# Performance work log

Measured on AMD Instinct MI355X. Metric: run time of the kernel, lower is better.

The kernel has to match this reference:

```python
import jax, jax.numpy as jnp
import numpy as np

MUL = 32      # multiplicity of each irrep type: 32x0e + 32x1o (dim = 32 + 96 = 128)
NSPEC = 10
NGRAPH = 16
EPS = 1e-5


def _split(x):
    # x: [N, 128] -> scalars [N, 32], vectors [N, 32, 3]
    return x[:, :MUL], x[:, MUL:].reshape(x.shape[0], MUL, 3)


def _cat(s, v):
    return jnp.concatenate([s, v.reshape(v.shape[0], MUL * 3)], axis=1)


def _irreps_linear(s, v, w0, w1, b0=None):
    # e3nn o3.Linear: per-irrep-type multiplicity mixing, /sqrt(fan_in), bias on scalars only
    inv = 1.0 / np.sqrt(MUL)
    s2 = s @ w0 * inv
    if b0 is not None:
        s2 = s2 + b0
    v2 = jnp.einsum('nuc,uw->nwc', v, w1) * inv
    return s2, v2


def _tensor_product(s1, v1, s2, v2, w000, w110, w011, w101):
    # SeparateWeightTensorProduct with per-path internal weights, lmax=1 paths:
    #   0e x 0e -> 0e, 1o x 1o -> 0e (CG = delta/sqrt(3)), 0e x 1o -> 1o, 1o x 0e -> 1o
    inv = 1.0 / np.sqrt(MUL * MUL)
    half = 1.0 / np.sqrt(2.0)  # two paths feed each output irrep
    out0 = (jnp.einsum('nu,nv,uvw->nw', s1, s2, w000)
            + jnp.einsum('nuc,nvc,uvw->nw', v1, v2, w110) / np.sqrt(3.0)) * (inv * half)
    out1 = (jnp.einsum('nu,nvc,uvw->nwc', s1, v2, w011)
            + jnp.einsum('nuc,nv,uvw->nwc', v1, s2, w101)) * (inv * half)
    return out0, out1


def _e3_layer_norm(s, v, batch, ln_w0, ln_b0, ln_w1):
    # per-graph equivariant layer norm: subtract mean on scalars, RMS-normalize each irrep field
    ones = jnp.ones(batch.shape, s.dtype)
    cnt = jnp.maximum(jax.ops.segment_sum(ones, batch, NGRAPH), 1.0)
    mean = jax.ops.segment_sum(s.sum(-1), batch, NGRAPH) / (cnt * MUL)
    s = s - mean[batch][:, None]
    n2s = jax.ops.segment_sum((s * s).sum(-1), batch, NGRAPH) / (cnt * MUL)
    s = s * jax.lax.rsqrt(n2s + EPS)[batch][:, None] * ln_w0 + ln_b0
    n2v = jax.ops.segment_sum((v * v).sum((-1, -2)), batch, NGRAPH) / (cnt * MUL)
    v = v * jax.lax.rsqrt(n2v + EPS)[batch][:, None, None] * ln_w1[None, :, None]
    return s, v


def setup_inputs() -> dict:
    key = jax.random.key(0)
    ks = jax.random.split(key, 24)
    N, B = 50000, 2
    rn = lambda k, sh: jax.random.normal(k, sh, dtype=jnp.float32)
    inp = {
        'node_feats_hidden': rn(ks[0], (B, N, MUL * 4)),
        'node_feats_up': rn(ks[1], (N, MUL * 4)),
        'hl_w0': rn(ks[2], (B, MUL, MUL)), 'hl_w1': rn(ks[3], (B, MUL, MUL)),
        'ul_w0': rn(ks[4], (B, MUL, MUL)), 'ul_w1': rn(ks[5], (B, MUL, MUL)),
        'tp_w000': rn(ks[6], (B, MUL, MUL, MUL)), 'tp_w110': rn(ks[7], (B, MUL, MUL, MUL)),
        'tp_w011': rn(ks[8], (B, MUL, MUL, MUL)), 'tp_w101': rn(ks[9], (B, MUL, MUL, MUL)),
        'lp_w0': rn(ks[10], (B, MUL, MUL)), 'lp_b0': jnp.zeros((B, MUL), jnp.float32),
        'lp_w1': rn(ks[11], (B, MUL, MUL)),
        'sc_w0': rn(ks[12], (B, MUL, NSPEC, MUL)), 'sc_w1': rn(ks[13], (B, MUL, NSPEC, MUL)),
        'ln_w0': jnp.ones((B, MUL), jnp.float32), 'ln_b0': jnp.zeros((B, MUL), jnp.float32),
        'ln_w1': jnp.ones((B, MUL), jnp.float32),
        'sk_w0': rn(ks[14], (B, MUL, MUL)), 'sk_b0': jnp.zeros((B, MUL), jnp.float32),
        'sk_w1': rn(ks[15], (B, MUL, MUL)),
        'node_species': jax.random.randint(ks[16], (N,), 0, NSPEC),
        'batch': jnp.sort(jax.random.randint(ks[17], (N,), 0, NGRAPH)),
    }
    return inp


def reference(node_feats_hidden, node_feats_up, hl_w0, hl_w1, ul_w0, ul_w1,
              tp_w000, tp_w110, tp_w011, tp_w101, lp_w0, lp_b0, lp_w1,
              sc_w0, sc_w1, ln_w0, ln_b0, ln_w1, sk_w0, sk_b0, sk_w1,
              node_species, batch):
    oh = jax.nn.one_hot(node_species, NSPEC, dtype=node_feats_up.dtype)
    inv_sc = 1.0 / np.sqrt(MUL * NSPEC)
    up = node_feats_up
    outs = []
    for b in range(node_feats_hidden.shape[0]):  # num_interactions blocks (fixed, small)
        sh, vh = _split(node_feats_hidden[b])
        su, vu = _split(up)
        shp, vhp = _irreps_linear(sh, vh, hl_w0[b], hl_w1[b])
        sup, vup = _irreps_linear(su, vu, ul_w0[b], ul_w1[b])
        z0, z1 = _tensor_product(shp, vhp, sup, vup,
                                 tp_w000[b], tp_w110[b], tp_w011[b], tp_w101[b])
        z0, z1 = _irreps_linear(z0, z1, lp_w0[b], lp_w1[b], lp_b0[b])
        # self connection: FullyConnectedTensorProduct(hidden, one-hot '10x0e', out)
        z0 = z0 + jnp.einsum('nu,nv,uvw->nw', sh, oh, sc_w0[b]) * inv_sc
        z1 = z1 + jnp.einsum('nuc,nv,uvw->nwc', vh, oh, sc_w1[b]) * inv_sc
        z0, z1 = _e3_layer_norm(z0, z1, batch, ln_w0[b], ln_b0[b], ln_w1[b])
        sk0, sk1 = _irreps_linear(sh, vh, sk_w0[b], sk_w1[b], sk_b0[b])
        out = _cat(z0 + sk0, z1 + sk1)
        outs.append(out)
        up = out  # next block consumes this block's output as node_feats_up
    return jnp.stack(outs)
```

## Files before the change

kernel.cpp:

```cpp
#include <hip/hip_runtime.h>
#include <math.h>

#define MULT 32
#define NSPEC 10
#define NGRAPH 16
#define NBANK 64
#define NCBANK 16
#define INV_SC 0.05590169943749474f
#define INV32S 0.17677669529663687f

typedef unsigned short u16;
typedef __bf16 v8bf __attribute__((ext_vector_type(8)));
typedef float v4f __attribute__((ext_vector_type(4)));
typedef unsigned int v4u_t __attribute__((ext_vector_type(4)));

__device__ __forceinline__ u16 f2bf(float f) {
    unsigned int u = __builtin_bit_cast(unsigned int, f);
    unsigned int r = u + 0x7fffu + ((u >> 16) & 1u);
    return (u16)(r >> 16);
}

__device__ __forceinline__ v8bf frag16(const u16* p) {
    return __builtin_bit_cast(v8bf, *(const v4u_t*)p);
}

#define MFMA(a, b, c) __builtin_amdgcn_mfma_f32_16x16x32_bf16(a, b, c, 0, 0, 0)

__global__ void zero_kernel(float* __restrict__ p, int n) {
    int i = blockIdx.x * 256 + threadIdx.x;
    if (i < n) p[i] = 0.0f;
}

__global__ void count_kernel(const int* __restrict__ batch, float* __restrict__ cntb, int N) {
    __shared__ int bins[NGRAPH];
    int t = threadIdx.x;
    if (t < NGRAPH) bins[t] = 0;
    __syncthreads();
    int i = blockIdx.x * 256 + t;
    if (i < N) atomicAdd(&bins[batch[i]], 1);
    __syncthreads();
    int bank = blockIdx.x & (NCBANK - 1);
    if (t < NGRAPH && bins[t] > 0) atomicAdd(&cntb[bank * NGRAPH + t], (float)bins[t]);
}

__global__ void stageA_kernel(const float* __restrict__ w000, const float* __restrict__ w110,
                              const float* __restrict__ w011, const float* __restrict__ w101,
                              const float* __restrict__ lp0, const float* __restrict__ lp1,
                              float* __restrict__ tmp1) {
    int gid = blockIdx.x * 256 + threadIdx.x;
    int tslot = gid >> 15;
    int e = gid & 32767;
    int z = e & 31;
    int uv = e >> 5;
    int b = tslot >> 2, path = tslot & 3;
    const float* W = (path == 0 ? w000 : path == 1 ? w110 : path == 2 ? w011 : w101) + b * 32768;
    const float* L = ((path == 0 || path == 1) ? lp0 : lp1) + b * 1024;
    float scale = (path == 1) ? (1.0f / (8192.0f * 1.7320508075688772f)) : (1.0f / 8192.0f);
    const float* wr = W + uv * 32;
    float acc = 0.0f;
    for (int w = 0; w < 32; ++w) acc += wr[w] * L[w * 32 + z];
    tmp1[gid] = acc * scale;
}

__global__ void stageB_kernel(const float* __restrict__ ul0, const float* __restrict__ ul1,
                              const float* __restrict__ tmp1, float* __restrict__ tmp2) {
    int gid = blockIdx.x * 256 + threadIdx.x;
    int tslot = gid >> 15;
    int e = gid & 32767;
    int z = e & 31;
    int bb = (e >> 5) & 31;
    int u = e >> 10;
    int b = tslot >> 2, path = tslot & 3;
    const float* U = ((path == 0 || path == 3) ? ul0 : ul1) + b * 1024;
    const float* in = tmp1 + (size_t)tslot * 32768 + u * 1024 + z;
    float acc = 0.0f;
    for (int v = 0; v < 32; ++v) acc += U[bb * 32 + v] * in[v * 32];
    tmp2[gid] = acc;
}

__global__ void stageC_kernel(const float* __restrict__ hl0, const float* __restrict__ hl1,
                              const float* __restrict__ tmp2, float* __restrict__ Weff) {
    int gid = blockIdx.x * 256 + threadIdx.x;
    int tslot = gid >> 15;
    int e = gid & 32767;
    int z = e & 31;
    int bb = (e >> 5) & 31;
    int a = e >> 10;
    int b = tslot >> 2, path = tslot & 3;
    const float* H = ((path == 0 || path == 2) ? hl0 : hl1) + b * 1024;
    const float* in = tmp2 + (size_t)tslot * 32768 + bb * 32 + z;
    float acc = 0.0f;
    for (int u = 0; u < 32; ++u) acc += H[a * 32 + u] * in[u * 1024];
    Weff[gid] = acc;
}

__global__ void pack_kernel(const float* __restrict__ Weff,
                            const float* __restrict__ sc_w0, const float* __restrict__ sc_w1,
                            u16* __restrict__ packs, int total) {
    int gid = blockIdx.x * 256 + threadIdx.x;
    if (gid >= total) return;
    int b = gid / 151552;
    int e = gid - b * 151552;
    float v;
    if (e < 131072) {
        int which = e >> 15;
        int e2 = e & 32767;
        int k = e2 & 31;
        int z = (e2 >> 5) & 31;
        int hi = e2 >> 10;
        int path = (which == 0) ? 0 : (which == 1) ? 2 : (which == 2) ? 3 : 1;
        int a  = (which < 2) ? k  : hi;
        int bb = (which < 2) ? hi : k;
        v = Weff[(size_t)((b * 4 + path) * 32 + a) * 1024 + bb * 32 + z];
    } else {
        int e2 = e - 131072;
        int which = e2 / 10240;
        int e3 = e2 - which * 10240;
        int s = e3 >> 10, z = (e3 >> 5) & 31, a = e3 & 31;
        const float* S = which ? sc_w1 : sc_w0;
        v = S[(size_t)b * 10240 + a * 320 + s * 32 + z] * INV_SC;
    }
    packs[gid] = f2bf(v);
}

__attribute__((amdgpu_waves_per_eu(4)))
__global__ __launch_bounds__(256)
void tp_kernel(const float* __restrict__ hidden_b, const float* __restrict__ up,
               const u16* __restrict__ pk,
               const float* __restrict__ lp_b0,
               const int* __restrict__ species, const int* __restrict__ batch,
               float* __restrict__ S1b, float* __restrict__ S2b, float* __restrict__ V2b,
               float* __restrict__ zout, int N) {
    constexpr int OFF_000 = 0, OFF_011 = 32768, OFF_101 = 65536, OFF_110 = 98304;
    constexpr int OFF_SC0 = 131072, OFF_SC1 = 141312;

    __shared__ __align__(16) char smem[24576];
    __shared__ int spec_l[16];
    __shared__ int bat_l[16];
    __shared__ float gs1[NGRAPH], gs2[NGRAPH], gv2[NGRAPH];

    u16* sh_bf = (u16*)smem;
    u16* su_bf = (u16*)(smem + 1280);
    u16* vu_bf = (u16*)(smem + 2560);
    u16* vh_bf = (u16*)(smem + 6400);
    float* suT = (float*)(smem + 10240);
    float* vuT = (float*)(smem + 12288);
    float* vhT = (float*)(smem + 18432);
    float* red = (float*)smem;

    const int t = threadIdx.x;
    const int w = t >> 6, lane = t & 63, quad = lane >> 4, c16 = lane & 15;
    const int n0 = blockIdx.x * 16;
    const int nvalid = min(16, N - n0);

    if (t < NGRAPH) { gs1[t] = 0.f; gs2[t] = 0.f; gv2[t] = 0.f; }
    if (t < 16) {
        spec_l[t] = (t < nvalid) ? species[n0 + t] : -1;
        bat_l[t]  = (t < nvalid) ? batch[n0 + t] : 0;
    }
    for (int i = t; i < 2048; i += 256) {
        int n = i >> 7, col = i & 127;
        float hv = 0.f, uv = 0.f;
        if (n < nvalid) {
            hv = hidden_b[(size_t)(n0 + n) * 128 + col];
            uv = up[(size_t)(n0 + n) * 128 + col];
        }
        if (col < 32) {
            sh_bf[n * 40 + col] = f2bf(hv); su_bf[n * 40 + col] = f2bf(uv);
            suT[col * 16 + n] = uv;
        } else {
            int idx = col - 32, c = idx % 3, a = idx / 3;
            vh_bf[(c * 16 + n) * 40 + a] = f2bf(hv);
            vu_bf[(c * 16 + n) * 40 + a] = f2bf(uv);
            vhT[(c * 32 + a) * 16 + n] = hv;
            vuT[(c * 32 + a) * 16 + n] = uv;
        }
    }
    __syncthreads();

    const v4f z4 = {0.f, 0.f, 0.f, 0.f};
    v4f o0[2];
    v4f o1[3][2];
    o0[0] = z4; o0[1] = z4;
#pragma unroll
    for (int c = 0; c < 3; ++c) { o1[c][0] = z4; o1[c][1] = z4; }

    v8bf a_sh = frag16(sh_bf + c16 * 40 + quad * 8);

    {
        const u16* Wb0 = pk + OFF_000 + (w * 256 + c16) * 32 + quad * 8;
        const u16* Wb1 = pk + OFF_011 + (w * 256 + c16) * 32 + quad * 8;
#pragma unroll 2
        for (int th = 0; th < 8; ++th) {
            int bb = w * 8 + th;
            v8bf fa0 = frag16(Wb0 + (th * 2) * 512);
            v8bf fa1 = frag16(Wb0 + (th * 2 + 1) * 512);
            v8bf fb0 = frag16(Wb1 + (th * 2) * 512);
            v8bf fb1 = frag16(Wb1 + (th * 2 + 1) * 512);
            v4f ys = *(const v4f*)(suT + bb * 16 + quad * 4);
            v4f C0 = MFMA(a_sh, fa0, z4);
            v4f C1 = MFMA(a_sh, fa1, z4);
            v4f D0 = MFMA(a_sh, fb0, z4);
            v4f D1 = MFMA(a_sh, fb1, z4);
#pragma unroll
            for (int r = 0; r < 4; ++r) {
                o0[0][r] += C0[r] * ys[r];
                o0[1][r] += C1[r] * ys[r];
            }
#pragma unroll
            for (int c = 0; c < 3; ++c) {
                v4f yv = *(const v4f*)(vuT + (c * 32 + bb) * 16 + quad * 4);
#pragma unroll
                for (int r = 0; r < 4; ++r) {
                    o1[c][0][r] += D0[r] * yv[r];
                    o1[c][1][r] += D1[r] * yv[r];
                }
            }
        }
    }
    {
        v8bf a_su = frag16(su_bf + c16 * 40 + quad * 8);
        v8bf av0 = frag16(vu_bf + (0 * 16 + c16) * 40 + quad * 8);
        v8bf av1 = frag16(vu_bf + (1 * 16 + c16) * 40 + quad * 8);
        v8bf av2 = frag16(vu_bf + (2 * 16 + c16) * 40 + quad * 8);
        const u16* Wb2 = pk + OFF_101 + (w * 256 + c16) * 32 + quad * 8;
        const u16* Wb3 = pk + OFF_110 + (w * 256 + c16) * 32 + quad * 8;
#pragma unroll 2
        for (int th = 0; th < 8; ++th) {
            int aa = w * 8 + th;
            v8bf fp0 = frag16(Wb2 + (th * 2) * 512);
            v8bf fp1 = frag16(Wb2 + (th * 2 + 1) * 512);
            v8bf fq0 = frag16(Wb3 + (th * 2) * 512);
            v8bf fq1 = frag16(Wb3 + (th * 2 + 1) * 512);
            v4f y0 = *(const v4f*)(vhT + (0 * 32 + aa) * 16 + quad * 4);
            v4f y1 = *(const v4f*)(vhT + (1 * 32 + aa) * 16 + quad * 4);
            v4f y2 = *(const v4f*)(vhT + (2 * 32 + aa) * 16 + quad * 4);
            v4f C0 = MFMA(a_su, fp0, z4);
            v4f C1 = MFMA(a_su, fp1, z4);
#pragma unroll
            for (int r = 0; r < 4; ++r) {
                o1[0][0][r] += C0[r] * y0[r]; o1[0][1][r] += C1[r] * y0[r];
                o1[1][0][r] += C0[r] * y1[r]; o1[1][1][r] += C1[r] * y1[r];
                o1[2][0][r] += C0[r] * y2[r]; o1[2][1][r] += C1[r] * y2[r];
            }
            v4f E00 = MFMA(av0, fq0, z4), E01 = MFMA(av0, fq1, z4);
            v4f E10 = MFMA(av1, fq0, z4), E11 = MFMA(av1, fq1, z4);
            v4f E20 = MFMA(av2, fq0, z4), E21 = MFMA(av2, fq1, z4);
#pragma unroll
            for (int r = 0; r < 4; ++r) {
                o0[0][r] += E00[r] * y0[r] + E10[r] * y1[r] + E20[r] * y2[r];
                o0[1][r] += E01[r] * y0[r] + E11[r] * y1[r] + E21[r] * y2[r];
            }
        }
    }
    {
        const int s0 = (w < 2) ? w * 3 : 6 + (w - 2) * 2;
        const int ns = (w < 2) ? 3 : 2;
        v8bf zf = __builtin_bit_cast(v8bf, (v4u_t){0u, 0u, 0u, 0u});
        int sp = spec_l[c16];
        v8bf a_vh0 = frag16(vh_bf + (0 * 16 + c16) * 40 + quad * 8);
        v8bf a_vh1 = frag16(vh_bf + (1 * 16 + c16) * 40 + quad * 8);
        v8bf a_vh2 = frag16(vh_bf + (2 * 16 + c16) * 40 + quad * 8);
        for (int si = s0; si < s0 + ns; ++si) {
            bool m = (sp == si);
            v8bf ash_m = m ? a_sh : zf;
            v8bf am0 = m ? a_vh0 : zf;
            v8bf am1 = m ? a_vh1 : zf;
            v8bf am2 = m ? a_vh2 : zf;
#pragma unroll
            for (int zh = 0; zh < 2; ++zh) {
                int boff = (si * 32 + zh * 16 + c16) * 32 + quad * 8;
                v8bf bf0 = frag16(pk + OFF_SC0 + boff);
                v8bf bf1 = frag16(pk + OFF_SC1 + boff);
                o0[zh] = MFMA(ash_m, bf0, o0[zh]);
                o1[0][zh] = MFMA(am0, bf1, o1[0][zh]);
                o1[1][zh] = MFMA(am1, bf1, o1[1][zh]);
                o1[2][zh] = MFMA(am2, bf1, o1[2][zh]);
            }
        }
    }

    __syncthreads();
    if (w < 2) {
#pragma unroll
        for (int r = 0; r < 4; ++r) {
            int n = quad * 4 + r;
            float* row = red + (w * 16 + n) * 132;
            row[c16]      = o0[0][r];
            row[16 + c16] = o0[1][r];
#pragma unroll
            for (int c = 0; c < 3; ++c) {
                row[32 + c16 * 3 + c]        = o1[c][0][r];
                row[32 + (16 + c16) * 3 + c] = o1[c][1][r];
            }
        }
    }
    __syncthreads();
    if (w >= 2) {
#pragma unroll
        for (int r = 0; r < 4; ++r) {
            int n = quad * 4 + r;
            float* row = red + ((w - 2) * 16 + n) * 132;
            row[c16]      += o0[0][r];
            row[16 + c16] += o0[1][r];
#pragma unroll
            for (int c = 0; c < 3; ++c) {
                row[32 + c16 * 3 + c]        += o1[c][0][r];
                row[32 + (16 + c16) * 3 + c] += o1[c][1][r];
            }
        }
    }
    __syncthreads();
    {
        int n = t >> 4, seg = t & 15;
        v4f sa = z4, sb = z4;
#pragma unroll
        for (int ww = 0; ww < 2; ++ww) {
            const float* rp = red + (ww * 16 + n) * 132 + seg * 8;
            sa += *(const v4f*)rp;
            sb += *(const v4f*)(rp + 4);
        }
        float s1p = 0.f, s2p = 0.f, v2p = 0.f;
        if (seg < 4) {
            sa += *(const v4f*)(lp_b0 + seg * 8);
            sb += *(const v4f*)(lp_b0 + seg * 8 + 4);
            s1p = sa[0] + sa[1] + sa[2] + sa[3] + sb[0] + sb[1] + sb[2] + sb[3];
            s2p = sa[0]*sa[0] + sa[1]*sa[1] + sa[2]*sa[2] + sa[3]*sa[3]
                + sb[0]*sb[0] + sb[1]*sb[1] + sb[2]*sb[2] + sb[3]*sb[3];
        } else {
            v2p = sa[0]*sa[0] + sa[1]*sa[1] + sa[2]*sa[2] + sa[3]*sa[3]
                + sb[0]*sb[0] + sb[1]*sb[1] + sb[2]*sb[2] + sb[3]*sb[3];
        }
        if (n < nvalid) {
            float* op = zout + (size_t)(n0 + n) * 128 + seg * 8;
            *(v4f*)op = sa;
            *(v4f*)(op + 4) = sb;
        }
#pragma unroll
        for (int off = 8; off >= 1; off >>= 1) {
            s1p += __shfl_xor(s1p, off, 16);
            s2p += __shfl_xor(s2p, off, 16);
            v2p += __shfl_xor(v2p, off, 16);
        }
        if (seg == 0 && n < nvalid) {
            int g = bat_l[n];
            atomicAdd(&gs1[g], s1p);
            atomicAdd(&gs2[g], s2p);
            atomicAdd(&gv2[g], v2p);
        }
    }
    __syncthreads();
    {
        const int bank = blockIdx.x & (NBANK - 1);
        if (t < NGRAPH) {
            if (gs1[t] != 0.f) atomicAdd(&S1b[bank * NGRAPH + t], gs1[t]);
            if (gs2[t] != 0.f) atomicAdd(&S2b[bank * NGRAPH + t], gs2[t]);
            if (gv2[t] != 0.f) atomicAdd(&V2b[bank * NGRAPH + t], gv2[t]);
        }
    }
}

__global__ __launch_bounds__(256)
void norm_kernel(const float* __restrict__ hidden_b, float* __restrict__ out_b,
                 const float* __restrict__ skw0, const float* __restrict__ skb0,
                 const float* __restrict__ skw1,
                 const float* __restrict__ lnw0, const float* __restrict__ lnb0,
                 const float* __restrict__ lnw1,
                 const int* __restrict__ batch,
                 const float* __restrict__ S1b, const float* __restrict__ S2b,
                 const float* __restrict__ V2b, const float* __restrict__ cntb, int N) {
    __shared__ __align__(16) float sh_l[8][32];
    __shared__ __align__(16) float vh_l[8][96];
    __shared__ float stat_s[3][NGRAPH];
    __shared__ float cnt_s[NGRAPH];
    const int t = threadIdx.x, z = t & 31, nl = t >> 5;
    const int n0 = blockIdx.x * 8;
    for (int i = t; i < 8 * 128; i += 256) {
        int n = i >> 7, col = i & 127;
        float v = (n0 + n < N) ? hidden_b[(size_t)(n0 + n) * 128 + col] : 0.f;
        if (col < 32) sh_l[n][col] = v; else vh_l[n][col - 32] = v;
    }
    if (t < 48) {
        int arr = t >> 4, g = t & 15;
        const float* base = (arr == 0) ? S1b : (arr == 1) ? S2b : V2b;
        float s = 0.f;
        for (int k = 0; k < NBANK; ++k) s += base[k * NGRAPH + g];
        stat_s[arr][g] = s;
    } else if (t < 64) {
        int g = t - 48;
        float c = 0.f;
        for (int k = 0; k < NCBANK; ++k) c += cntb[k * NGRAPH + g];
        cnt_s[g] = c;
    }
    __syncthreads();
    const int n = n0 + nl;
    if (n >= N) return;

    float sk0 = 0.f, s1 = 0.f, s2 = 0.f, s3 = 0.f;
    for (int a = 0; a < 32; ++a) {
        float w0 = skw0[a * 32 + z];
        float w1 = skw1[a * 32 + z];
        sk0 += sh_l[nl][a] * w0;
        s1 += vh_l[nl][a * 3 + 0] * w1;
        s2 += vh_l[nl][a * 3 + 1] * w1;
        s3 += vh_l[nl][a * 3 + 2] * w1;
    }
    int g = batch[n];
    float cM = fmaxf(cnt_s[g], 1.0f) * 32.0f;
    float mean = stat_s[0][g] / cM;
    float var = fmaxf(stat_s[1][g] / cM - mean * mean, 0.0f);
    float rs = rsqrtf(var + 1e-5f);
    float rv = rsqrtf(fmaxf(stat_s[2][g] / cM, 0.0f) + 1e-5f);

    size_t base = (size_t)n * 128;
    float z0 = out_b[base + z];
    out_b[base + z] = (z0 - mean) * rs * lnw0[z] + lnb0[z] + sk0 * INV32S + skb0[z];
    float lw = lnw1[z] * rv;
    float x0 = out_b[base + 32 + z * 3 + 0];
    float x1 = out_b[base + 32 + z * 3 + 1];
    float x2 = out_b[base + 32 + z * 3 + 2];
    out_b[base + 32 + z * 3 + 0] = x0 * lw + s1 * INV32S;
    out_b[base + 32 + z * 3 + 1] = x1 * lw + s2 * INV32S;
    out_b[base + 32 + z * 3 + 2] = x2 * lw + s3 * INV32S;
}

extern "C" void kernel_launch(void* const* d_in, const int* in_sizes, int n_in,
                              void* d_out, int out_size, void* d_ws, size_t ws_size,
                              hipStream_t stream) {
    const float* hidden = (const float*)d_in[0];
    const float* up0    = (const float*)d_in[1];
    const float* hl_w0  = (const float*)d_in[2];
    const float* hl_w1  = (const float*)d_in[3];
    const float* ul_w0  = (const float*)d_in[4];
    const float* ul_w1  = (const float*)d_in[5];
    const float* w000   = (const float*)d_in[6];
    const float* w110   = (const float*)d_in[7];
    const float* w011   = (const float*)d_in[8];
    const float* w101   = (const float*)d_in[9];
    const float* lp_w0  = (const float*)d_in[10];
    const float* lp_b0  = (const float*)d_in[11];
    const float* lp_w1  = (const float*)d_in[12];
    const float* sc_w0  = (const float*)d_in[13];
    const float* sc_w1  = (const float*)d_in[14];
    const float* ln_w0  = (const float*)d_in[15];
    const float* ln_b0  = (const float*)d_in[16];
    const float* ln_w1  = (const float*)d_in[17];
    const float* sk_w0  = (const float*)d_in[18];
    const float* sk_b0  = (const float*)d_in[19];
    const float* sk_w1  = (const float*)d_in[20];
    const int* species  = (const int*)d_in[21];
    const int* batch    = (const int*)d_in[22];
    float* out = (float*)d_out;

    const int N = in_sizes[21];
    const int B = in_sizes[0] / (N * 128);

    float* ws = (float*)d_ws;
    float* tmp1 = ws;
    float* tmp2 = tmp1 + (size_t)B * 4 * 32768;
    float* cntb = tmp2 + (size_t)B * 4 * 32768;
    float* S1b = cntb + NCBANK * NGRAPH;
    float* S2b = S1b + (size_t)B * NBANK * NGRAPH;
    float* V2b = S2b + (size_t)B * NBANK * NGRAPH;
    int statn = NCBANK * NGRAPH + 3 * B * NBANK * NGRAPH;

    zero_kernel<<<(statn + 255) / 256, 256, 0, stream>>>(cntb, statn);
    count_kernel<<<(N + 255) / 256, 256, 0, stream>>>(batch, cntb, N);

    int nb = B * 4 * 32768 / 256;
    stageA_kernel<<<nb, 256, 0, stream>>>(w000, w110, w011, w101, lp_w0, lp_w1, tmp1);
    stageB_kernel<<<nb, 256, 0, stream>>>(ul_w0, ul_w1, tmp1, tmp2);
    stageC_kernel<<<nb, 256, 0, stream>>>(hl_w0, hl_w1, tmp2, tmp1);

    u16* packs = (u16*)tmp2;
    int ptotal = B * 151552;
    pack_kernel<<<(ptotal + 255) / 256, 256, 0, stream>>>(tmp1, sc_w0, sc_w1, packs, ptotal);

    for (int b = 0; b < B; ++b) {
        const float* up = (b == 0) ? up0 : out + (size_t)(b - 1) * N * 128;
        const u16* pb = packs + (size_t)b * 151552;
        tp_kernel<<<(N + 15) / 16, 256, 0, stream>>>(
            hidden + (size_t)b * N * 128, up, pb,
            lp_b0 + b * MULT, species, batch,
            S1b + (size_t)b * NBANK * NGRAPH, S2b + (size_t)b * NBANK * NGRAPH,
            V2b + (size_t)b * NBANK * NGRAPH,
            out + (size_t)b * N * 128, N);
        norm_kernel<<<(N + 7) / 8, 256, 0, stream>>>(
            hidden + (size_t)b * N * 128, out + (size_t)b * N * 128,
            sk_w0 + b * 1024, sk_b0 + b * MULT, sk_w1 + b * 1024,
            ln_w0 + b * MULT, ln_b0 + b * MULT, ln_w1 + b * MULT,
            batch, S1b + (size_t)b * NBANK * NGRAPH, S2b + (size_t)b * NBANK * NGRAPH,
            V2b + (size_t)b * NBANK * NGRAPH, cntb, N);
    }
}
```

Baseline: 383.9 us.

## Fuse previous block's layer-norm and skip into next block's TP kernel

Block b's layer norm, skip linear and output writeback now run inside block b+1's tp_kernel prologue. The normalized result is used directly as that block's up input and written back to global memory. Only the last block still launches the separate norm_kernel. This removes one kernel launch and one full read/write pass of the intermediate output. In exchange, each TP block computes the per-node skip linear with scalar loops and uses 16KB more shared memory, which may lower occupancy.

```diff
diff --git a/kernel.cpp b/kernel.cpp
--- a/kernel.cpp
+++ b/kernel.cpp
@@ -130,14 +130,27 @@
                const float* __restrict__ lp_b0,
                const int* __restrict__ species, const int* __restrict__ batch,
                float* __restrict__ S1b, float* __restrict__ S2b, float* __restrict__ V2b,
-               float* __restrict__ zout, int N) {
+               float* __restrict__ zout, int N,
+               int do_norm,
+               const float* __restrict__ ph,
+               float* __restrict__ po,
+               const float* __restrict__ skw0p, const float* __restrict__ skb0p,
+               const float* __restrict__ skw1p,
+               const float* __restrict__ lnw0p, const float* __restrict__ lnb0p,
+               const float* __restrict__ lnw1p,
+               const float* __restrict__ S1p, const float* __restrict__ S2p,
+               const float* __restrict__ V2p, const float* __restrict__ cntb) {
     constexpr int OFF_000 = 0, OFF_011 = 32768, OFF_101 = 65536, OFF_110 = 98304;
     constexpr int OFF_SC0 = 131072, OFF_SC1 = 141312;
 
     __shared__ __align__(16) char smem[24576];
+    __shared__ __align__(16) float rawH[2048];
+    __shared__ __align__(16) float rawZ[2048];
     __shared__ int spec_l[16];
     __shared__ int bat_l[16];
     __shared__ float gs1[NGRAPH], gs2[NGRAPH], gv2[NGRAPH];
+    __shared__ float stat_s[3][NGRAPH];
+    __shared__ float cnt_s[NGRAPH];
 
     u16* sh_bf = (u16*)smem;
     u16* su_bf = (u16*)(smem + 1280);
@@ -158,25 +171,101 @@
         spec_l[t] = (t < nvalid) ? species[n0 + t] : -1;
         bat_l[t]  = (t < nvalid) ? batch[n0 + t] : 0;
     }
-    for (int i = t; i < 2048; i += 256) {
-        int n = i >> 7, col = i & 127;
-        float hv = 0.f, uv = 0.f;
-        if (n < nvalid) {
-            hv = hidden_b[(size_t)(n0 + n) * 128 + col];
-            uv = up[(size_t)(n0 + n) * 128 + col];
-        }
-        if (col < 32) {
-            sh_bf[n * 40 + col] = f2bf(hv); su_bf[n * 40 + col] = f2bf(uv);
-            suT[col * 16 + n] = uv;
-        } else {
-            int idx = col - 32, c = idx % 3, a = idx / 3;
-            vh_bf[(c * 16 + n) * 40 + a] = f2bf(hv);
-            vu_bf[(c * 16 + n) * 40 + a] = f2bf(uv);
-            vhT[(c * 32 + a) * 16 + n] = hv;
-            vuT[(c * 32 + a) * 16 + n] = uv;
-        }
-    }
-    __syncthreads();
+
+    if (do_norm) {
+        for (int i = t; i < 2048; i += 256) {
+            int n = i >> 7, col = i & 127;
+            bool ok = n < nvalid;
+            float hv = ok ? hidden_b[(size_t)(n0 + n) * 128 + col] : 0.f;
+            rawH[i] = ok ? ph[(size_t)(n0 + n) * 128 + col] : 0.f;
+            rawZ[i] = ok ? po[(size_t)(n0 + n) * 128 + col] : 0.f;
+            if (col < 32) {
+                sh_bf[n * 40 + col] = f2bf(hv);
+            } else {
+                int idx = col - 32, c = idx % 3, a = idx / 3;
+                vh_bf[(c * 16 + n) * 40 + a] = f2bf(hv);
+                vhT[(c * 32 + a) * 16 + n] = hv;
+            }
+        }
+        if (t < 48) {
+            int arr = t >> 4, g = t & 15;
+            const float* base = (arr == 0) ? S1p : (arr == 1) ? S2p : V2p;
+            float s = 0.f;
+            for (int k = 0; k < NBANK; ++k) s += base[k * NGRAPH + g];
+            stat_s[arr][g] = s;
+        } else if (t < 64) {
+            int g = t - 48;
+            float c = 0.f;
+            for (int k = 0; k < NCBANK; ++k) c += cntb[k * NGRAPH + g];
+            cnt_s[g] = c;
+        }
+        __syncthreads();
+        {
+            int nl = t >> 4, zz = t & 15;
+            int g = bat_l[nl];
+            float cM = fmaxf(cnt_s[g], 1.0f) * 32.0f;
+            float mean = stat_s[0][g] / cM;
+            float var = fmaxf(stat_s[1][g] / cM - mean * mean, 0.0f);
+            float rs = rsqrtf(var + 1e-5f);
+            float rv = rsqrtf(fmaxf(stat_s[2][g] / cM, 0.0f) + 1e-5f);
+            float* H = rawH + nl * 128;
+            float* Z = rawZ + nl * 128;
+#pragma unroll
+            for (int dz = 0; dz < 2; ++dz) {
+                int z = zz * 2 + dz;
+                float sk0 = 0.f, s1 = 0.f, s2 = 0.f, s3 = 0.f;
+                for (int a = 0; a < 32; ++a) {
+                    float w0 = skw0p[a * 32 + z];
+                    float w1 = skw1p[a * 32 + z];
+                    sk0 += H[a] * w0;
+                    s1 += H[32 + a * 3 + 0] * w1;
+                    s2 += H[32 + a * 3 + 1] * w1;
+                    s3 += H[32 + a * 3 + 2] * w1;
+                }
+                float z0v = Z[z];
+                Z[z] = (z0v - mean) * rs * lnw0p[z] + lnb0p[z] + sk0 * INV32S + skb0p[z];
+                float lw = lnw1p[z] * rv;
+                Z[32 + z * 3 + 0] = Z[32 + z * 3 + 0] * lw + s1 * INV32S;
+                Z[32 + z * 3 + 1] = Z[32 + z * 3 + 1] * lw + s2 * INV32S;
+                Z[32 + z * 3 + 2] = Z[32 + z * 3 + 2] * lw + s3 * INV32S;
+            }
+        }
+        __syncthreads();
+        for (int i = t; i < 2048; i += 256) {
+            int n = i >> 7, col = i & 127;
+            float uv = rawZ[i];
+            if (col < 32) {
+                su_bf[n * 40 + col] = f2bf(uv);
+                suT[col * 16 + n] = uv;
+            } else {
+                int idx = col - 32, c = idx % 3, a = idx / 3;
+                vu_bf[(c * 16 + n) * 40 + a] = f2bf(uv);
+                vuT[(c * 32 + a) * 16 + n] = uv;
+            }
+            if (n < nvalid) po[(size_t)(n0 + n) * 128 + col] = uv;
+        }
+        __syncthreads();
+    } else {
+        for (int i = t; i < 2048; i += 256) {
+            int n = i >> 7, col = i & 127;
+            float hv = 0.f, uv = 0.f;
+            if (n < nvalid) {
+                hv = hidden_b[(size_t)(n0 + n) * 128 + col];
+                uv = up[(size_t)(n0 + n) * 128 + col];
+            }
+            if (col < 32) {
+                sh_bf[n * 40 + col] = f2bf(hv); su_bf[n * 40 + col] = f2bf(uv);
+                suT[col * 16 + n] = uv;
+            } else {
+                int idx = col - 32, c = idx % 3, a = idx / 3;
+                vh_bf[(c * 16 + n) * 40 + a] = f2bf(hv);
+                vu_bf[(c * 16 + n) * 40 + a] = f2bf(uv);
+                vhT[(c * 32 + a) * 16 + n] = hv;
+                vuT[(c * 32 + a) * 16 + n] = uv;
+            }
+        }
+        __syncthreads();
+    }
 
     const v4f z4 = {0.f, 0.f, 0.f, 0.f};
     v4f o0[2];
@@ -477,14 +566,32 @@
     pack_kernel<<<(ptotal + 255) / 256, 256, 0, stream>>>(tmp1, sc_w0, sc_w1, packs, ptotal);
 
     for (int b = 0; b < B; ++b) {
-        const float* up = (b == 0) ? up0 : out + (size_t)(b - 1) * N * 128;
         const u16* pb = packs + (size_t)b * 151552;
-        tp_kernel<<<(N + 15) / 16, 256, 0, stream>>>(
-            hidden + (size_t)b * N * 128, up, pb,
-            lp_b0 + b * MULT, species, batch,
-            S1b + (size_t)b * NBANK * NGRAPH, S2b + (size_t)b * NBANK * NGRAPH,
-            V2b + (size_t)b * NBANK * NGRAPH,
-            out + (size_t)b * N * 128, N);
+        if (b == 0) {
+            tp_kernel<<<(N + 15) / 16, 256, 0, stream>>>(
+                hidden, up0, pb, lp_b0, species, batch,
+                S1b, S2b, V2b, out, N,
+                0, hidden, out, sk_w0, sk_b0, sk_w1, ln_w0, ln_b0, ln_w1,
+                S1b, S2b, V2b, cntb);
+        } else {
+            int pbv = b - 1;
+            tp_kernel<<<(N + 15) / 16, 256, 0, stream>>>(
+                hidden + (size_t)b * N * 128, out + (size_t)pbv * N * 128, pb,
+                lp_b0 + b * MULT, species, batch,
+                S1b + (size_t)b * NBANK * NGRAPH, S2b + (size_t)b * NBANK * NGRAPH,
+                V2b + (size_t)b * NBANK * NGRAPH,
+                out + (size_t)b * N * 128, N,
+                1,
+                hidden + (size_t)pbv * N * 128,
+                out + (size_t)pbv * N * 128,
+                sk_w0 + pbv * 1024, sk_b0 + pbv * MULT, sk_w1 + pbv * 1024,
+                ln_w0 + pbv * MULT, ln_b0 + pbv * MULT, ln_w1 + pbv * MULT,
+                S1b + (size_t)pbv * NBANK * NGRAPH, S2b + (size_t)pbv * NBANK * NGRAPH,
+                V2b + (size_t)pbv * NBANK * NGRAPH, cntb);
+        }
+    }
+    {
+        int b = B - 1;
         norm_kernel<<<(N + 7) / 8, 256, 0, stream>>>(
             hidden + (size_t)b * N * 128, out + (size_t)b * N * 128,
             sk_w0 + b * 1024, sk_b0 + b * MULT, sk_w1 + b * 1024,
```

Result: slower. 434.9 us (+13.3%).

## Fuse weight-precompute stages A+B via shared memory and stage C with packing

Applied to the files above, without the earlier changes.

Merges the first two weight-contraction stages into one kernel that keeps the per-u weight slab, the linear matrices and the intermediate in shared memory. It also fuses the third contraction with the bf16 packing step, writing packed weights directly. This cuts the weight preprocessing from four launches to two and drops a full fp32 intermediate round trip. The node-level tp and norm kernels, which dominate the run time, are unchanged.

```diff
diff --git a/kernel.cpp b/kernel.cpp
--- a/kernel.cpp
+++ b/kernel.cpp
@@ -43,84 +43,88 @@
     if (t < NGRAPH && bins[t] > 0) atomicAdd(&cntb[bank * NGRAPH + t], (float)bins[t]);
 }
 
-__global__ void stageA_kernel(const float* __restrict__ w000, const float* __restrict__ w110,
-                              const float* __restrict__ w011, const float* __restrict__ w101,
-                              const float* __restrict__ lp0, const float* __restrict__ lp1,
-                              float* __restrict__ tmp1) {
+__global__ __launch_bounds__(256)
+void stageAB_kernel(const float* __restrict__ w000, const float* __restrict__ w110,
+                    const float* __restrict__ w011, const float* __restrict__ w101,
+                    const float* __restrict__ lp0, const float* __restrict__ lp1,
+                    const float* __restrict__ ul0, const float* __restrict__ ul1,
+                    float* __restrict__ tmp2) {
+    __shared__ __align__(16) float Wrow[1024];
+    __shared__ __align__(16) float Lm[1024];
+    __shared__ __align__(16) float Um[1024];
+    __shared__ __align__(16) float T1[1024];
+
+    const int t = threadIdx.x;
+    const int tslot = blockIdx.x >> 5;
+    const int u = blockIdx.x & 31;
+    const int b = tslot >> 2, path = tslot & 3;
+    const float* W = (path == 0 ? w000 : path == 1 ? w110 : path == 2 ? w011 : w101)
+                     + b * 32768 + u * 1024;
+    const float* L = ((path == 0 || path == 1) ? lp0 : lp1) + b * 1024;
+    const float* U = ((path == 0 || path == 3) ? ul0 : ul1) + b * 1024;
+    const float scale = (path == 1) ? (1.0f / (8192.0f * 1.7320508075688772f))
+                                    : (1.0f / 8192.0f);
+
+    *(v4f*)&Wrow[t * 4] = *(const v4f*)(W + t * 4);
+    *(v4f*)&Lm[t * 4]   = *(const v4f*)(L + t * 4);
+    *(v4f*)&Um[t * 4]   = *(const v4f*)(U + t * 4);
+    __syncthreads();
+
+#pragma unroll
+    for (int j = 0; j < 4; ++j) {
+        int idx = t + 256 * j;
+        int v = idx >> 5, z = idx & 31;
+        float acc = 0.0f;
+        for (int w = 0; w < 32; ++w) acc += Wrow[v * 32 + w] * Lm[w * 32 + z];
+        T1[v * 32 + z] = acc * scale;
+    }
+    __syncthreads();
+
+    float* outp = tmp2 + (size_t)tslot * 32768 + u * 1024;
+#pragma unroll
+    for (int j = 0; j < 4; ++j) {
+        int idx = t + 256 * j;
+        int bb = idx >> 5, z = idx & 31;
+        float acc = 0.0f;
+        for (int v = 0; v < 32; ++v) acc += Um[bb * 32 + v] * T1[v * 32 + z];
+        outp[idx] = acc;
+    }
+}
+
+__global__ __launch_bounds__(256)
+void stageCpack_kernel(const float* __restrict__ hl0, const float* __restrict__ hl1,
+                       const float* __restrict__ tmp2,
+                       const float* __restrict__ sc_w0, const float* __restrict__ sc_w1,
+                       u16* __restrict__ packs, int wtotal, int total) {
     int gid = blockIdx.x * 256 + threadIdx.x;
-    int tslot = gid >> 15;
-    int e = gid & 32767;
-    int z = e & 31;
-    int uv = e >> 5;
-    int b = tslot >> 2, path = tslot & 3;
-    const float* W = (path == 0 ? w000 : path == 1 ? w110 : path == 2 ? w011 : w101) + b * 32768;
-    const float* L = ((path == 0 || path == 1) ? lp0 : lp1) + b * 1024;
-    float scale = (path == 1) ? (1.0f / (8192.0f * 1.7320508075688772f)) : (1.0f / 8192.0f);
-    const float* wr = W + uv * 32;
-    float acc = 0.0f;
-    for (int w = 0; w < 32; ++w) acc += wr[w] * L[w * 32 + z];
-    tmp1[gid] = acc * scale;
-}
-
-__global__ void stageB_kernel(const float* __restrict__ ul0, const float* __restrict__ ul1,
-                              const float* __restrict__ tmp1, float* __restrict__ tmp2) {
-    int gid = blockIdx.x * 256 + threadIdx.x;
-    int tslot = gid >> 15;
-    int e = gid & 32767;
-    int z = e & 31;
-    int bb = (e >> 5) & 31;
-    int u = e >> 10;
-    int b = tslot >> 2, path = tslot & 3;
-    const float* U = ((path == 0 || path == 3) ? ul0 : ul1) + b * 1024;
-    const float* in = tmp1 + (size_t)tslot * 32768 + u * 1024 + z;
-    float acc = 0.0f;
-    for (int v = 0; v < 32; ++v) acc += U[bb * 32 + v] * in[v * 32];
-    tmp2[gid] = acc;
-}
-
-__global__ void stageC_kernel(const float* __restrict__ hl0, const float* __restrict__ hl1,
-                              const float* __restrict__ tmp2, float* __restrict__ Weff) {
-    int gid = blockIdx.x * 256 + threadIdx.x;
-    int tslot = gid >> 15;
-    int e = gid & 32767;
-    int z = e & 31;
-    int bb = (e >> 5) & 31;
-    int a = e >> 10;
-    int b = tslot >> 2, path = tslot & 3;
-    const float* H = ((path == 0 || path == 2) ? hl0 : hl1) + b * 1024;
-    const float* in = tmp2 + (size_t)tslot * 32768 + bb * 32 + z;
-    float acc = 0.0f;
-    for (int u = 0; u < 32; ++u) acc += H[a * 32 + u] * in[u * 1024];
-    Weff[gid] = acc;
-}
-
-__global__ void pack_kernel(const float* __restrict__ Weff,
-                            const float* __restrict__ sc_w0, const float* __restrict__ sc_w1,
-                            u16* __restrict__ packs, int total) {
-    int gid = blockIdx.x * 256 + threadIdx.x;
-    if (gid >= total) return;
-    int b = gid / 151552;
-    int e = gid - b * 151552;
-    float v;
-    if (e < 131072) {
-        int which = e >> 15;
-        int e2 = e & 32767;
-        int k = e2 & 31;
-        int z = (e2 >> 5) & 31;
-        int hi = e2 >> 10;
-        int path = (which == 0) ? 0 : (which == 1) ? 2 : (which == 2) ? 3 : 1;
-        int a  = (which < 2) ? k  : hi;
-        int bb = (which < 2) ? hi : k;
-        v = Weff[(size_t)((b * 4 + path) * 32 + a) * 1024 + bb * 32 + z];
-    } else {
-        int e2 = e - 131072;
-        int which = e2 / 10240;
-        int e3 = e2 - which * 10240;
+    if (gid < wtotal) {
+        int tslot = gid >> 15;
+        int e = gid & 32767;
+        int z = e & 31;
+        int bb = (e >> 5) & 31;
+        int a = e >> 10;
+        int b = tslot >> 2, path = tslot & 3;
+        const float* H = ((path == 0 || path == 2) ? hl0 : hl1) + b * 1024;
+        const float* in = tmp2 + (size_t)tslot * 32768 + bb * 32 + z;
+        float acc = 0.0f;
+        for (int u = 0; u < 32; ++u) acc += H[a * 32 + u] * in[u * 1024];
+        int off, e2;
+        if (path == 0)      { off = 0;      e2 = bb * 1024 + z * 32 + a; }
+        else if (path == 2) { off = 32768;  e2 = bb * 1024 + z * 32 + a; }
+        else if (path == 3) { off = 65536;  e2 = a * 1024 + z * 32 + bb; }
+        else                { off = 98304;  e2 = a * 1024 + z * 32 + bb; }
+        packs[(size_t)b * 151552 + off + e2] = f2bf(acc);
+    } else if (gid < total) {
+        int gid2 = gid - wtotal;
+        int b = gid2 / 20480;
+        int e3p = gid2 - b * 20480;
+        int which = e3p / 10240;
+        int e3 = e3p - which * 10240;
         int s = e3 >> 10, z = (e3 >> 5) & 31, a = e3 & 31;
         const float* S = which ? sc_w1 : sc_w0;
-        v = S[(size_t)b * 10240 + a * 320 + s * 32 + z] * INV_SC;
-    }
-    packs[gid] = f2bf(v);
+        float v = S[(size_t)b * 10240 + a * 320 + s * 32 + z] * INV_SC;
+        packs[(size_t)b * 151552 + 131072 + which * 10240 + e3] = f2bf(v);
+    }
 }
 
 __attribute__((amdgpu_waves_per_eu(4)))
@@ -456,8 +460,8 @@
     const int B = in_sizes[0] / (N * 128);
 
     float* ws = (float*)d_ws;
-    float* tmp1 = ws;
-    float* tmp2 = tmp1 + (size_t)B * 4 * 32768;
+    u16* packs = (u16*)ws;
+    float* tmp2 = ws + (size_t)B * 4 * 32768;
     float* cntb = tmp2 + (size_t)B * 4 * 32768;
     float* S1b = cntb + NCBANK * NGRAPH;
     float* S2b = S1b + (size_t)B * NBANK * NGRAPH;
@@ -467,14 +471,13 @@
     zero_kernel<<<(statn + 255) / 256, 256, 0, stream>>>(cntb, statn);
     count_kernel<<<(N + 255) / 256, 256, 0, stream>>>(batch, cntb, N);
 
-    int nb = B * 4 * 32768 / 256;
-    stageA_kernel<<<nb, 256, 0, stream>>>(w000, w110, w011, w101, lp_w0, lp_w1, tmp1);
-    stageB_kernel<<<nb, 256, 0, stream>>>(ul_w0, ul_w1, tmp1, tmp2);
-    stageC_kernel<<<nb, 256, 0, stream>>>(hl_w0, hl_w1, tmp2, tmp1);
-
-    u16* packs = (u16*)tmp2;
-    int ptotal = B * 151552;
-    pack_kernel<<<(ptotal + 255) / 256, 256, 0, stream>>>(tmp1, sc_w0, sc_w1, packs, ptotal);
+    stageAB_kernel<<<B * 4 * 32, 256, 0, stream>>>(
+        w000, w110, w011, w101, lp_w0, lp_w1, ul_w0, ul_w1, tmp2);
+
+    int wtotal = B * 4 * 32768;
+    int total = wtotal + B * 20480;
+    stageCpack_kernel<<<(total + 255) / 256, 256, 0, stream>>>(
+        hl_w0, hl_w1, tmp2, sc_w0, sc_w1, packs, wtotal, total);
 
     for (int b = 0; b < B; ++b) {
         const float* up = (b == 0) ? up0 : out + (size_t)(b - 1) * N * 128;
```

Result: no change. 378.9 us (-1.3%).
